# Performance work log

Measured on AMD Instinct MI355X. Metric: run time of the kernel, lower is better.

Reference implementation:

```python
import jax, jax.numpy as jnp
import numpy as np

K = 12
CHUNK = 1024
N_LAYERS = 4
WIDTH = 192
COND = 64
PE_DIM = 3 * 8 * 2 + 3  # 51
OUT_SCALE = 0.01
BIG = 1e9


def _build_knn(x, k=K, chunk=CHUNK):
    """Brute-force kNN, row-chunked like the TF double-chunked version.
    x: (N,3) float32 -> (N,k) int32 neighbor indices (self excluded)."""
    n = x.shape[0]
    x = x.astype(jnp.float32)
    x_sq = jnp.sum(x * x, axis=1)  # (N,)
    col_ids = jnp.arange(n, dtype=jnp.int32)
    starts = jnp.arange(0, n, chunk, dtype=jnp.int32)

    def one_chunk(start):
        xc = jax.lax.dynamic_slice(x, (start, 0), (chunk, 3))        # (chunk,3)
        sq_c = jax.lax.dynamic_slice(x_sq, (start,), (chunk,))       # (chunk,)
        d = sq_c[:, None] + x_sq[None, :] - 2.0 * (xc @ x.T)         # (chunk,N)
        d = jnp.maximum(d, 0.0)
        rows = start + jnp.arange(chunk, dtype=jnp.int32)
        d = d + jnp.where(rows[:, None] == col_ids[None, :], BIG, 0.0)  # exclude self
        _, idx = jax.lax.top_k(-d, k)                                 # smallest distances
        return idx.astype(jnp.int32)

    idx = jax.lax.map(one_chunk, starts)  # (n/chunk, chunk, k)
    return idx.reshape(n, k)


def _fourier(x, Bs):
    """concat_k [sin(xB_k), cos(xB_k)] + x  -> (N, PE_DIM)."""
    feats = []
    for B in Bs:
        xb = x @ B  # (N,8)
        feats.append(jnp.sin(xb))
        feats.append(jnp.cos(xb))
    feats.append(x)
    return jnp.concatenate(feats, axis=-1)


def setup_inputs() -> dict:
    key = jax.random.key(0)
    ks = jax.random.split(key, 16)
    n = 32768
    x = jax.random.normal(ks[0], (n, 3), dtype=jnp.float32)
    z = jax.random.normal(ks[1], (COND,), dtype=jnp.float32)
    sigmas = (1.0, 10.0, 50.0)
    B0 = jax.random.normal(ks[2], (3, 8), dtype=jnp.float32) * sigmas[0]
    B1 = jax.random.normal(ks[3], (3, 8), dtype=jnp.float32) * sigmas[1]
    B2 = jax.random.normal(ks[4], (3, 8), dtype=jnp.float32) * sigmas[2]
    in_total = PE_DIM + COND  # 115
    s = 0.05
    Wp = jax.random.normal(ks[5], (in_total, WIDTH), dtype=jnp.float32) * s
    bp = jnp.zeros((WIDTH,), dtype=jnp.float32)
    mix_dim = WIDTH + WIDTH + 6  # feat + agg + rel_feat
    Wl = jax.random.normal(ks[6], (N_LAYERS, mix_dim, WIDTH), dtype=jnp.float32) * s
    bl = jnp.zeros((N_LAYERS, WIDTH), dtype=jnp.float32)
    # FiLM: kernel ~zeros, gamma bias=ones, beta bias=zeros (perturbed slightly)
    Wg = jax.random.normal(ks[7], (N_LAYERS, COND, WIDTH), dtype=jnp.float32) * 0.01
    bg = jnp.ones((N_LAYERS, WIDTH), dtype=jnp.float32)
    Wb = jax.random.normal(ks[8], (N_LAYERS, COND, WIDTH), dtype=jnp.float32) * 0.01
    bb = jnp.zeros((N_LAYERS, WIDTH), dtype=jnp.float32)
    Wout = jax.random.normal(ks[9], (WIDTH, 3), dtype=jnp.float32) * s
    bout = jnp.zeros((3,), dtype=jnp.float32)
    return {"x": x, "z": z, "B0": B0, "B1": B1, "B2": B2,
            "Wp": Wp, "bp": bp, "Wl": Wl, "bl": bl,
            "Wg": Wg, "bg": bg, "Wb": Wb, "bb": bb,
            "Wout": Wout, "bout": bout}


def reference(x, z, B0, B1, B2, Wp, bp, Wl, bl, Wg, bg, Wb, bb, Wout, bout):
    n = x.shape[0]
    knn_idx = _build_knn(x)                     # (N,K) int32
    pe = _fourier(x, (B0, B1, B2))              # (N,51)
    zb = jnp.broadcast_to(z[None, :], (n, COND))
    feat = jnp.concatenate([pe, zb], axis=-1)   # (N,115)
    h = jax.nn.silu(feat @ Wp + bp)             # (N,WIDTH)
    # precompute relative-coordinate stats (same for all layers)
    nbr_coords = x[knn_idx]                     # (N,K,3)
    rel = nbr_coords - x[:, None, :]
    rel_feat = jnp.concatenate([rel.mean(axis=1), rel.std(axis=1)], axis=-1)  # (N,6)
    for li in range(N_LAYERS):
        nbr = h[knn_idx]                        # (N,K,WIDTH) gather
        agg = nbr.mean(axis=1)                  # (N,WIDTH)
        mix = jnp.concatenate([h, agg, rel_feat], axis=-1)  # (N,390)
        h = jax.nn.silu(mix @ Wl[li] + bl[li])
        gamma = z @ Wg[li] + bg[li]             # (WIDTH,)
        beta = z @ Wb[li] + bb[li]
        h = h * gamma[None, :] + beta[None, :]  # FiLM
    out = (h @ Wout + bout) * OUT_SCALE         # (N,3)
    return out
```

## Files before the change

kernel.cpp:

```cpp
#include <hip/hip_runtime.h>
#include <math.h>

#define WIDTH 192
#define KNN 12
#define G 64
#define NCELLS (G * G * G)
#define SMAX 8

#define CE(a, b) { double _lo = fmin(a, b); double _hi = fmax(a, b); a = _lo; b = _hi; }
#define INSERT12(key) { \
    b11 = fmin(b11, key); \
    CE(b10, b11); CE(b9, b10); CE(b8, b9); CE(b7, b8); CE(b6, b7); \
    CE(b5, b6);  CE(b4, b5); CE(b3, b4); CE(b2, b3); CE(b1, b2); CE(b0, b1); }
#define DECL12 double b0,b1,b2,b3,b4,b5,b6,b7,b8,b9,b10,b11
#define INIT12 { b0=__hiloint2double(0x7F7FFFFF,0);  b1=__hiloint2double(0x7F7FFFFF,1); \
    b2=__hiloint2double(0x7F7FFFFF,2);  b3=__hiloint2double(0x7F7FFFFF,3); \
    b4=__hiloint2double(0x7F7FFFFF,4);  b5=__hiloint2double(0x7F7FFFFF,5); \
    b6=__hiloint2double(0x7F7FFFFF,6);  b7=__hiloint2double(0x7F7FFFFF,7); \
    b8=__hiloint2double(0x7F7FFFFF,8);  b9=__hiloint2double(0x7F7FFFFF,9); \
    b10=__hiloint2double(0x7F7FFFFF,10); b11=__hiloint2double(0x7F7FFFFF,11); }

#define MERGE_STAGE(m) { \
    double pb11 = shflx_d(b11, m), pb10 = shflx_d(b10, m), pb9 = shflx_d(b9, m); \
    double pb8  = shflx_d(b8, m),  pb7  = shflx_d(b7, m),  pb6 = shflx_d(b6, m); \
    double pb5  = shflx_d(b5, m),  pb4  = shflx_d(b4, m),  pb3 = shflx_d(b3, m); \
    double pb2  = shflx_d(b2, m),  pb1  = shflx_d(b1, m),  pb0 = shflx_d(b0, m); \
    double c12 = pb3, c13 = pb2, c14 = pb1, c15 = pb0; \
    b4 = fmin(b4, pb11); b5 = fmin(b5, pb10); b6 = fmin(b6, pb9);  b7 = fmin(b7, pb8); \
    b8 = fmin(b8, pb7);  b9 = fmin(b9, pb6);  b10 = fmin(b10, pb5); b11 = fmin(b11, pb4); \
    CE(b0, b8);  CE(b1, b9);  CE(b2, b10); CE(b3, b11); \
    CE(b4, c12); CE(b5, c13); CE(b6, c14); CE(b7, c15); \
    CE(b0, b4);  CE(b1, b5);  CE(b2, b6);  CE(b3, b7); \
    CE(b8, c12); CE(b9, c13); CE(b10, c14); CE(b11, c15); \
    CE(b0, b2);  CE(b1, b3);  CE(b4, b6);  CE(b5, b7); \
    CE(b8, b10); CE(b9, b11); \
    CE(b0, b1);  CE(b2, b3);  CE(b4, b5);  CE(b6, b7); \
    CE(b8, b9);  CE(b10, b11); }

__device__ inline unsigned encf(float f) {
    unsigned u = __float_as_uint(f);
    return (u & 0x80000000u) ? ~u : (u | 0x80000000u);
}
__device__ inline float decf(unsigned u) {
    return (u & 0x80000000u) ? __uint_as_float(u & 0x7fffffffu) : __uint_as_float(~u);
}
__device__ inline int cellc(float v, float mn, float invh) {
    int c = (int)((v - mn) * invh);
    return min(max(c, 0), G - 1);
}
__device__ inline double shflx_d(double v, int m) {
    int lo = __shfl_xor(__double2loint(v), m, 64);
    int hi = __shfl_xor(__double2hiint(v), m, 64);
    return __hiloint2double(hi, lo);
}

__global__ __launch_bounds__(256) void precompute_kernel(
    const float* __restrict__ z, const float* __restrict__ Wp, const float* __restrict__ bp,
    const float* __restrict__ Wg, const float* __restrict__ bg,
    const float* __restrict__ Wb, const float* __restrict__ bb,
    float* __restrict__ bias0, float* __restrict__ gammaB, float* __restrict__ betaB)
{
    __shared__ float zs[64];
    int t = threadIdx.x;
    if (t < 64) zs[t] = z[t];
    __syncthreads();
    if (t < WIDTH) {
        float acc = bp[t];
        for (int k = 0; k < 64; ++k) acc += zs[k] * Wp[(51 + k) * WIDTH + t];
        bias0[t] = acc;
        for (int l = 0; l < 4; ++l) {
            float g = bg[l * WIDTH + t];
            float b = bb[l * WIDTH + t];
            for (int k = 0; k < 64; ++k) {
                g += zs[k] * Wg[(l * 64 + k) * WIDTH + t];
                b += zs[k] * Wb[(l * 64 + k) * WIDTH + t];
            }
            gammaB[l * WIDTH + t] = g;
            betaB[l * WIDTH + t] = b;
        }
    }
}

__global__ __launch_bounds__(256) void init_kernel(
    unsigned* __restrict__ bb, unsigned* __restrict__ counts,
    unsigned long long* __restrict__ rowmask)
{
    int i = blockIdx.x * 256 + threadIdx.x;
    if (i < 3) bb[i] = 0xFFFFFFFFu;
    else if (i < 6) bb[i] = 0u;
    counts[i] = 0u;
    if (i < G * G) rowmask[i] = 0ull;
}

__global__ __launch_bounds__(256) void bbox_kernel(
    const float* __restrict__ x, unsigned* __restrict__ bb, int n)
{
    int i = blockIdx.x * 256 + threadIdx.x;
    unsigned emin[3], emax[3];
#pragma unroll
    for (int a = 0; a < 3; ++a) { unsigned e = encf(x[i * 3 + a]); emin[a] = e; emax[a] = e; }
#pragma unroll
    for (int o = 32; o; o >>= 1) {
#pragma unroll
        for (int a = 0; a < 3; ++a) {
            emin[a] = min(emin[a], (unsigned)__shfl_xor((int)emin[a], o, 64));
            emax[a] = max(emax[a], (unsigned)__shfl_xor((int)emax[a], o, 64));
        }
    }
    if ((threadIdx.x & 63) == 0) {
#pragma unroll
        for (int a = 0; a < 3; ++a) {
            atomicMin(&bb[a], emin[a]);
            atomicMax(&bb[3 + a], emax[a]);
        }
    }
}

__global__ __launch_bounds__(256) void hist_kernel(
    const float* __restrict__ x, const unsigned* __restrict__ bb,
    unsigned* __restrict__ counts, unsigned long long* __restrict__ rowmask, int n)
{
    int i = blockIdx.x * 256 + threadIdx.x;
    float mnx = decf(bb[0]), mny = decf(bb[1]), mnz = decf(bb[2]);
    float ivx = (float)G / (decf(bb[3]) - mnx);
    float ivy = (float)G / (decf(bb[4]) - mny);
    float ivz = (float)G / (decf(bb[5]) - mnz);
    int cx = cellc(x[i * 3 + 0], mnx, ivx);
    int cy = cellc(x[i * 3 + 1], mny, ivy);
    int cz = cellc(x[i * 3 + 2], mnz, ivz);
    atomicAdd(&counts[(cz * G + cy) * G + cx], 1u);
    atomicOr(&rowmask[cz * G + cy], 1ull << cx);
}

__global__ __launch_bounds__(256) void scan1_kernel(
    const unsigned* __restrict__ counts, unsigned* __restrict__ offs,
    unsigned* __restrict__ bsums)
{
    __shared__ unsigned s[256];
    int b = blockIdx.x, t = threadIdx.x;
    unsigned base = (unsigned)b * 1024 + t * 4;
    unsigned v[4], sum = 0;
#pragma unroll
    for (int k = 0; k < 4; ++k) { v[k] = counts[base + k]; sum += v[k]; }
    s[t] = sum; __syncthreads();
    for (int off = 1; off < 256; off <<= 1) {
        unsigned xv = (t >= off) ? s[t - off] : 0u;
        __syncthreads();
        s[t] += xv;
        __syncthreads();
    }
    unsigned excl = s[t] - sum;
    if (t == 255) bsums[b] = s[255];
    unsigned run = excl;
#pragma unroll
    for (int k = 0; k < 4; ++k) { offs[base + k] = run; run += v[k]; }
}

__global__ __launch_bounds__(256) void scan3_kernel(
    unsigned* __restrict__ offs, const unsigned* __restrict__ bsums,
    unsigned* __restrict__ cursors, int n)
{
    __shared__ unsigned s[256];
    int b = blockIdx.x, t = threadIdx.x;
    s[t] = (t < b) ? bsums[t] : 0u;
    __syncthreads();
    for (int off = 128; off; off >>= 1) {
        if (t < off) s[t] += s[t + off];
        __syncthreads();
    }
    unsigned add = s[0];
    unsigned base = (unsigned)b * 1024 + t * 4;
#pragma unroll
    for (int k = 0; k < 4; ++k) {
        unsigned v = offs[base + k] + add;
        offs[base + k] = v;
        cursors[base + k] = v;
    }
    if (b == 255 && t == 255) offs[NCELLS] = (unsigned)n;
}

__global__ __launch_bounds__(256) void scatter_kernel(
    const float* __restrict__ x, const unsigned* __restrict__ bb,
    unsigned* __restrict__ cursors, float4* __restrict__ sorted,
    unsigned* __restrict__ inv, int n)
{
    int i = blockIdx.x * 256 + threadIdx.x;
    float mnx = decf(bb[0]), mny = decf(bb[1]), mnz = decf(bb[2]);
    float ivx = (float)G / (decf(bb[3]) - mnx);
    float ivy = (float)G / (decf(bb[4]) - mny);
    float ivz = (float)G / (decf(bb[5]) - mnz);
    float x0 = x[i * 3 + 0], x1 = x[i * 3 + 1], x2 = x[i * 3 + 2];
    int cx = cellc(x0, mnx, ivx);
    int cy = cellc(x1, mny, ivy);
    int cz = cellc(x2, mnz, ivz);
    unsigned pos = atomicAdd(&cursors[(cz * G + cy) * G + cx], 1u);
    sorted[pos] = make_float4(x0, x1, x2, __int_as_float(i));
    inv[i] = pos;
}

__global__ __launch_bounds__(64) void knn_grid_kernel(
    const float4* __restrict__ sorted, const unsigned* __restrict__ offs,
    const unsigned long long* __restrict__ rowmask,
    const unsigned* __restrict__ bb, const float* __restrict__ x,
    const unsigned* __restrict__ inv,
    unsigned short* __restrict__ knn, float* __restrict__ relf, int n)
{
    const int l = threadIdx.x;
    const int l32 = l & 31;
    const int g32 = l >> 5;
    const int b = blockIdx.x;
    const int nch = n >> 6;
    const int ch = b >> 5, posb = b & 31;
    const int fch = (ch & 1) ? (nch - 1 - (ch >> 1)) : (ch >> 1);
    const int p = fch * 64 + posb * 2 + g32;

    float mnx = decf(bb[0]), mny = decf(bb[1]), mnz = decf(bb[2]);
    float mxx = decf(bb[3]), mxy = decf(bb[4]), mxz = decf(bb[5]);
    float hx = (mxx - mnx) / G, hy = (mxy - mny) / G, hz = (mxz - mnz) / G;
    float ivx = (float)G / (mxx - mnx);
    float ivy = (float)G / (mxy - mny);
    float ivz = (float)G / (mxz - mnz);

    float4 q = sorted[p];
    float xi = q.x, yi = q.y, zi = q.z;
    int iorig = __float_as_int(q.w);
    float sqi = fmaf(zi, zi, fmaf(yi, yi, xi * xi));
    int cx = cellc(xi, mnx, ivx), cy = cellc(yi, mny, ivy), cz = cellc(zi, mnz, ivz);
    float fx = (xi - mnx) - cx * hx;
    float fy = (yi - mny) - cy * hy;
    float fz = (zi - mnz) - cz * hz;

    DECL12; INIT12;
    float worst = 3.402823466e+38f;
    float worst_g = 3.402823466e+38f;
    int nc = 0;
    bool have12 = false;

    auto groupMinWorst = [&]() -> float {
        float wm = worst;
        wm = fminf(wm, __shfl_xor(wm, 1, 64));
        wm = fminf(wm, __shfl_xor(wm, 2, 64));
        wm = fminf(wm, __shfl_xor(wm, 4, 64));
        wm = fminf(wm, __shfl_xor(wm, 8, 64));
        wm = fminf(wm, __shfl_xor(wm, 16, 64));
        return wm;
    };

    auto lane12Bound = [&]() -> float {
        float v = __int_as_float(__double2hiint(b0));
#pragma unroll
        for (int k = 2; k <= 32; k <<= 1) {
#pragma unroll
            for (int j = k >> 1; j >= 1; j >>= 1) {
                float pv = __shfl_xor(v, j, 64);
                bool dir = ((l32 & k) == 0);
                bool lower = ((l32 & j) == 0);
                float mn = fminf(v, pv), mx = fmaxf(v, pv);
                v = (lower == dir) ? mn : mx;
            }
        }
        return __shfl(v, (l & 32) | 11, 64);
    };

    auto groupUnionD12 = [&]() -> float {
        double c0=b0,c1=b1,c2=b2,c3=b3,c4=b4,c5=b5,c6=b6,c7=b7,c8=b8,c9=b9,c10=b10,c11=b11;
        {
            double b0=c0,b1=c1,b2=c2,b3=c3,b4=c4,b5=c5,b6=c6,b7=c7,b8=c8,b9=c9,b10=c10,b11=c11;
#pragma unroll
            for (int m = 1; m <= 16; m <<= 1) MERGE_STAGE(m)
            return __int_as_float(__double2hiint(b11));
        }
    };

    auto scanRange = [&](int c0, int c1) {
        unsigned j0 = offs[c0], j1 = offs[c1 + 1];
        if (j0 >= j1) return;
        float4 c = sorted[j0];
        for (unsigned t = j0; t < j1; ++t) {
            unsigned tn = (t + 1 < j1) ? t + 1 : t;
            float4 nx = sorted[tn];
            float sqj = fmaf(c.z, c.z, fmaf(c.y, c.y, c.x * c.x));
            float dot = fmaf(zi, c.z, fmaf(yi, c.y, xi * c.x));
            float d = fmaf(-2.0f, dot, sqi + sqj);
            int jg = __float_as_int(c.w);
            if (d <= fminf(worst, worst_g) && jg != iorig) {
                d = fmaxf(d, 0.0f);
                double key = __hiloint2double(__float_as_int(d), jg);
                INSERT12(key);
                worst = __int_as_float(__double2hiint(b11));
                ++nc;
            }
            c = nx;
        }
    };

    auto scanStrided = [&](int c0, int c1, int sub, int step) {
        unsigned j0 = offs[c0], j1 = offs[c1 + 1];
        for (unsigned t = j0 + sub; t < j1; t += step) {
            float4 c = sorted[t];
            float sqj = fmaf(c.z, c.z, fmaf(c.y, c.y, c.x * c.x));
            float dot = fmaf(zi, c.z, fmaf(yi, c.y, xi * c.x));
            float d = fmaf(-2.0f, dot, sqi + sqj);
            int jg = __float_as_int(c.w);
            if (d <= fminf(worst, worst_g) && jg != iorig) {
                d = fmaxf(d, 0.0f);
                double key = __hiloint2double(__float_as_int(d), jg);
                INSERT12(key);
                worst = __int_as_float(__double2hiint(b11));
                ++nc;
            }
        }
    };

    auto doRow = [&](int s, int dz, int dy, int sub, int step) {
        int zz = cz + dz, yy = cy + dy;
        if (zz < 0 || zz >= G || yy < 0 || yy >= G) return;
        int row = zz * G + yy;
        unsigned long long rm = rowmask[row];
        if (rm == 0ull) return;
        int rb = row * G;
        int adz = dz < 0 ? -dz : dz, ady = dy < 0 ? -dy : dy;
        if (adz == s || ady == s) {
            int x0 = max(cx - s, 0), x1 = min(cx + s, G - 1);
            unsigned long long msk =
                ((x1 == 63) ? ~0ull : ((1ull << (x1 + 1)) - 1ull)) &
                ~((1ull << x0) - 1ull);
            unsigned long long mm = rm & msk;
            if (mm) {
                int c0 = __ffsll((unsigned long long)mm) - 1;
                int c1 = 63 - __clzll((long long)mm);
                if (step == 1) scanRange(rb + c0, rb + c1);
                else           scanStrided(rb + c0, rb + c1, sub, step);
            }
        } else {
            int xm = cx - s, xp = cx + s;
            if (xm >= 0 && ((rm >> xm) & 1ull)) {
                if (step == 1) scanRange(rb + xm, rb + xm);
                else           scanStrided(rb + xm, rb + xm, sub, step);
            }
            if (xp < G && ((rm >> xp) & 1ull)) {
                if (step == 1) scanRange(rb + xp, rb + xp);
                else           scanStrided(rb + xp, rb + xp, sub, step);
            }
        }
    };

    auto check12 = [&]() {
        if (!have12) {
            int ns = nc;
#pragma unroll
            for (int o = 1; o <= 16; o <<= 1) ns += __shfl_xor(ns, o, 64);
            have12 = (ns >= 12);
        }
    };

    bool done = false;
    for (int s = 0; s <= SMAX; ++s) {
        if (s > 0) {
            float bx = (s - 1) * hx + fminf(fx, hx - fx);
            float by = (s - 1) * hy + fminf(fy, hy - fy);
            float bz = (s - 1) * hz + fminf(fz, hz - fz);
            float bnd = fminf(bx, fminf(by, bz));
            float bnd2 = bnd * bnd;
            worst_g = fminf(worst_g, groupMinWorst());
            if (bnd2 > worst_g + 1e-4f) { done = true; break; }
            unsigned long long anyb =
                __ballot(__double2hiint(b0) != 0x7F7FFFFF);
            unsigned gm = (unsigned)(anyb >> (g32 << 5));
            if (__popc(gm) >= 12) {
                worst_g = fminf(worst_g, lane12Bound());
                if (bnd2 > worst_g + 1e-4f) { done = true; break; }
            }
            if (s >= 2) {
                check12();
                if (have12) {
                    worst_g = fminf(worst_g, groupUnionD12());
                    if (bnd2 > worst_g + 1e-4f) { done = true; break; }
                }
            }
        }
        if (s == 0) {
            int row = cz * G + cy;
            if ((rowmask[row] >> cx) & 1ull) {
                int rb = row * G;
                scanStrided(rb + cx, rb + cx, l32, 32);
            }
        } else {
            int w2 = 2 * s + 1;
            int nrows = w2 * w2;
            int lpr = 32 / nrows;
            if (lpr > 1) {
                int r = l32 / lpr, sub = l32 - r * lpr;
                if (r < nrows) {
                    int dz = r / w2 - s, dy = r - (r / w2) * w2 - s;
                    doRow(s, dz, dy, sub, lpr);
                }
            } else {
                float rcp = 1.0f / (float)w2;
                for (int r = l32; r < nrows; r += 32) {
                    int qd = (int)((float)r * rcp);
                    int rem = r - qd * w2;
                    if (rem < 0) { qd--; rem += w2; }
                    else if (rem >= w2) { qd++; rem -= w2; }
                    doRow(s, qd - s, rem - s, 0, 1);
                }
            }
        }
    }
    if (!done) {
        float bx = SMAX * hx + fminf(fx, hx - fx);
        float by = SMAX * hy + fminf(fy, hy - fy);
        float bz = SMAX * hz + fminf(fz, hz - fz);
        float bnd = fminf(bx, fminf(by, bz));
        float bnd2 = bnd * bnd;
        worst_g = fminf(worst_g, groupMinWorst());
        if (bnd2 > worst_g + 1e-4f) done = true;
        if (!done) {
            unsigned long long anyb =
                __ballot(__double2hiint(b0) != 0x7F7FFFFF);
            unsigned gm = (unsigned)(anyb >> (g32 << 5));
            if (__popc(gm) >= 12) {
                worst_g = fminf(worst_g, lane12Bound());
                if (bnd2 > worst_g + 1e-4f) done = true;
            }
        }
        if (!done) {
            check12();
            if (have12) {
                worst_g = fminf(worst_g, groupUnionD12());
                if (bnd2 > worst_g + 1e-4f) done = true;
            }
        }
    }
    if (!done) {
        INIT12;
        worst = 3.402823466e+38f;
        for (int base = 0; base < n; base += 256) {
            float4 cc[8];
#pragma unroll
            for (int r = 0; r < 8; ++r) cc[r] = sorted[base + l32 + r * 32];
#pragma unroll
            for (int r = 0; r < 8; ++r) {
                float4 c = cc[r];
                float sqj = fmaf(c.z, c.z, fmaf(c.y, c.y, c.x * c.x));
                float dot = fmaf(zi, c.z, fmaf(yi, c.y, xi * c.x));
                float d = fmaf(-2.0f, dot, sqi + sqj);
                int jg = __float_as_int(c.w);
                if (d <= fminf(worst, worst_g) && jg != iorig) {
                    d = fmaxf(d, 0.0f);
                    double key = __hiloint2double(__float_as_int(d), jg);
                    INSERT12(key);
                    worst = __int_as_float(__double2hiint(b11));
                }
            }
        }
    }

#pragma unroll
    for (int m = 1; m <= 16; m <<= 1) MERGE_STAGE(m)

    if (l32 == 0) {
        int idx[KNN];
        idx[0]=__double2loint(b0);  idx[1]=__double2loint(b1);  idx[2]=__double2loint(b2);
        idx[3]=__double2loint(b3);  idx[4]=__double2loint(b4);  idx[5]=__double2loint(b5);
        idx[6]=__double2loint(b6);  idx[7]=__double2loint(b7);  idx[8]=__double2loint(b8);
        idx[9]=__double2loint(b9);  idx[10]=__double2loint(b10); idx[11]=__double2loint(b11);

        float rx[KNN], ry[KNN], rz[KNN];
        float sx = 0.f, sy = 0.f, sz = 0.f;
#pragma unroll
        for (int s = 0; s < KNN; ++s) {
            int j = idx[s];
            knn[(size_t)p * KNN + s] = (unsigned short)inv[j];
            rx[s] = x[(size_t)j * 3 + 0] - xi;
            ry[s] = x[(size_t)j * 3 + 1] - yi;
            rz[s] = x[(size_t)j * 3 + 2] - zi;
            sx += rx[s]; sy += ry[s]; sz += rz[s];
        }
        float mx = sx / 12.0f, my = sy / 12.0f, mz = sz / 12.0f;
        float vx = 0.f, vy = 0.f, vz = 0.f;
#pragma unroll
        for (int s = 0; s < KNN; ++s) {
            float dx = rx[s] - mx, dy = ry[s] - my, dz = rz[s] - mz;
            vx += dx * dx; vy += dy * dy; vz += dz * dz;
        }
        float* rr = relf + (size_t)p * 8;
        rr[0] = mx; rr[1] = my; rr[2] = mz;
        rr[3] = sqrtf(vx / 12.0f); rr[4] = sqrtf(vy / 12.0f); rr[5] = sqrtf(vz / 12.0f);
        rr[6] = 0.0f; rr[7] = 0.0f;
    }
}

template <int MODE>
__global__ __launch_bounds__(256) void gemm_silu_kernel(
    const float* __restrict__ A0, const unsigned short* __restrict__ knnp,
    const float* __restrict__ Rel, const float4* __restrict__ sorted4,
    const float* __restrict__ Bf0, const float* __restrict__ Bf1,
    const float* __restrict__ Bf2,
    const float* __restrict__ W, const float* __restrict__ bias,
    const float* __restrict__ gamma, const float* __restrict__ beta,
    const float* __restrict__ Wout, const float* __restrict__ bout,
    float* __restrict__ hout, float* __restrict__ fout)
{
    __shared__ float As[16][68];
    __shared__ float Bs[16][196];
    __shared__ float wouts[576];
    const int tid = threadIdx.x;
    const int ty = tid >> 4, tx = tid & 15;
    const int m0 = blockIdx.x * 64;
    const int arow = tid >> 2, akoff = (tid & 3) * 4;
    const int bk = tid >> 4,  bc = (tid & 15) * 12;

    float acc[4][12] = {};
    const int NCH = (MODE == 0) ? 4 : 24;

    if (MODE == 2) {
        for (int e = tid; e < 576; e += 256) wouts[e] = Wout[e];
    }

    float qx = 0.f, qy = 0.f, qz = 0.f;
    if (MODE == 0) {
        float4 qq = sorted4[m0 + arow];
        qx = qq.x; qy = qq.y; qz = qq.z;
    }

    unsigned kf[6] = {0, 0, 0, 0, 0, 0};
    if (MODE != 0) {
        const unsigned* kp = (const unsigned*)(knnp + (size_t)(m0 + arow) * KNN);
#pragma unroll
        for (int w = 0; w < 6; ++w) kf[w] = kp[w];
    }

    auto loadA = [&](int ch) -> float4 {
        int k0 = ch * 16;
        if (MODE == 0) {
            int c0 = k0 + akoff;
            float v[4];
            if (c0 < 48) {
                int m = c0 >> 4, jb = c0 & 15;
                const float* B = (m == 0) ? Bf0 : (m == 1) ? Bf1 : Bf2;
                bool iscos = jb >= 8;
                int j0 = iscos ? jb - 8 : jb;
#pragma unroll
                for (int e = 0; e < 4; ++e) {
                    int j = j0 + e;
                    float arg = qx * B[j] + qy * B[8 + j] + qz * B[16 + j];
                    v[e] = iscos ? cosf(arg) : sinf(arg);
                }
            } else {
#pragma unroll
                for (int e = 0; e < 4; ++e) {
                    int c = c0 + e;
                    v[e] = (c == 48) ? qx : (c == 49) ? qy : (c == 50) ? qz : 0.0f;
                }
            }
            return make_float4(v[0], v[1], v[2], v[3]);
        } else if (k0 < 192) {
            return *(const float4*)&A0[(size_t)(m0 + arow) * 192 + k0 + akoff];
        } else {
            int c4 = (k0 - 192 + akoff) >> 2;
            const float4* h4 = (const float4*)A0;
            float4 s = make_float4(0.f, 0.f, 0.f, 0.f);
#pragma unroll
            for (int j = 0; j < KNN; ++j) {
                unsigned idx = (j & 1) ? (kf[j >> 1] >> 16) : (kf[j >> 1] & 0xFFFFu);
                float4 v = h4[(size_t)idx * 48 + c4];
                s.x += v.x; s.y += v.y; s.z += v.z; s.w += v.w;
            }
            const float r = 1.0f / 12.0f;
            return make_float4(s.x * r, s.y * r, s.z * r, s.w * r);
        }
    };

    float4 ra = loadA(0);
    const float* wr0 = &W[(size_t)bk * 192 + bc];
    float4 rb0 = *(const float4*)&wr0[0];
    float4 rb1 = *(const float4*)&wr0[4];
    float4 rb2 = *(const float4*)&wr0[8];

    for (int ch = 0; ch < NCH; ++ch) {
        As[akoff + 0][arow] = ra.x; As[akoff + 1][arow] = ra.y;
        As[akoff + 2][arow] = ra.z; As[akoff + 3][arow] = ra.w;
        *(float4*)&Bs[bk][bc + 0] = rb0;
        *(float4*)&Bs[bk][bc + 4] = rb1;
        *(float4*)&Bs[bk][bc + 8] = rb2;
        __syncthreads();
        if (ch + 1 < NCH) {
            ra = loadA(ch + 1);
            const float* wr = &W[(size_t)((ch + 1) * 16 + bk) * 192 + bc];
            rb0 = *(const float4*)&wr[0];
            rb1 = *(const float4*)&wr[4];
            rb2 = *(const float4*)&wr[8];
        }
#pragma unroll
        for (int k = 0; k < 16; ++k) {
            float4 a0 = *(const float4*)&As[k][ty * 4];
            float av[4] = {a0.x, a0.y, a0.z, a0.w};
            float4 q0 = *(const float4*)&Bs[k][tx * 12 + 0];
            float4 q1 = *(const float4*)&Bs[k][tx * 12 + 4];
            float4 q2 = *(const float4*)&Bs[k][tx * 12 + 8];
            float bv[12] = {q0.x, q0.y, q0.z, q0.w, q1.x, q1.y, q1.z, q1.w,
                            q2.x, q2.y, q2.z, q2.w};
#pragma unroll
            for (int a = 0; a < 4; ++a)
#pragma unroll
                for (int bcol = 0; bcol < 12; ++bcol)
                    acc[a][bcol] = fmaf(av[a], bv[bcol], acc[a][bcol]);
        }
        __syncthreads();
    }

    if (MODE != 0) {
        {
            int row = tid >> 2, cp = (tid & 3) * 2;
            float2 v = *(const float2*)&Rel[(size_t)(m0 + row) * 8 + cp];
            As[cp + 0][row] = v.x; As[cp + 1][row] = v.y;
        }
        {
            int k2 = tid >> 4, c = (tid & 15) * 12;
            if (k2 < 8) {
                int gk = 384 + k2; if (gk > 389) gk = 389;
                const float* wr = &W[(size_t)gk * 192 + c];
                *(float4*)&Bs[k2][c + 0] = *(const float4*)&wr[0];
                *(float4*)&Bs[k2][c + 4] = *(const float4*)&wr[4];
                *(float4*)&Bs[k2][c + 8] = *(const float4*)&wr[8];
            }
        }
        __syncthreads();
#pragma unroll
        for (int k = 0; k < 8; ++k) {
            float4 a0 = *(const float4*)&As[k][ty * 4];
            float av[4] = {a0.x, a0.y, a0.z, a0.w};
            float4 q0 = *(const float4*)&Bs[k][tx * 12 + 0];
            float4 q1 = *(const float4*)&Bs[k][tx * 12 + 4];
            float4 q2 = *(const float4*)&Bs[k][tx * 12 + 8];
            float bv[12] = {q0.x, q0.y, q0.z, q0.w, q1.x, q1.y, q1.z, q1.w,
                            q2.x, q2.y, q2.z, q2.w};
#pragma unroll
            for (int a = 0; a < 4; ++a)
#pragma unroll
                for (int bcol = 0; bcol < 12; ++bcol)
                    acc[a][bcol] = fmaf(av[a], bv[bcol], acc[a][bcol]);
        }
        __syncthreads();
    }

    float po[4][3] = {};
#pragma unroll
    for (int a = 0; a < 4; ++a) {
        int gi = m0 + ty * 4 + a;
        float res[12];
#pragma unroll
        for (int bcol = 0; bcol < 12; ++bcol) {
            int gc = tx * 12 + bcol;
            float v = acc[a][bcol] + bias[gc];
            float s = 1.0f / (1.0f + expf(-v));
            v = v * s;
            if (MODE != 0) v = v * gamma[gc] + beta[gc];
            res[bcol] = v;
        }
        if (MODE == 2) {
#pragma unroll
            for (int e = 0; e < 12; ++e) {
                int c = tx * 12 + e;
                po[a][0] = fmaf(res[e], wouts[c * 3 + 0], po[a][0]);
                po[a][1] = fmaf(res[e], wouts[c * 3 + 1], po[a][1]);
                po[a][2] = fmaf(res[e], wouts[c * 3 + 2], po[a][2]);
            }
        } else {
            float* orow = &hout[(size_t)gi * 192 + tx * 12];
            *(float4*)&orow[0] = make_float4(res[0], res[1], res[2], res[3]);
            *(float4*)&orow[4] = make_float4(res[4], res[5], res[6], res[7]);
            *(float4*)&orow[8] = make_float4(res[8], res[9], res[10], res[11]);
        }
    }

    if (MODE == 2) {
#pragma unroll
        for (int a = 0; a < 4; ++a)
#pragma unroll
            for (int j = 0; j < 3; ++j) {
                float v = po[a][j];
                v += __shfl_xor(v, 1, 64);
                v += __shfl_xor(v, 2, 64);
                v += __shfl_xor(v, 4, 64);
                v += __shfl_xor(v, 8, 64);
                po[a][j] = v;
            }
        if (tx == 0) {
#pragma unroll
            for (int a = 0; a < 4; ++a) {
                int gi = m0 + ty * 4 + a;
                int iorig = __float_as_int(sorted4[gi].w);
                fout[(size_t)iorig * 3 + 0] = (po[a][0] + bout[0]) * 0.01f;
                fout[(size_t)iorig * 3 + 1] = (po[a][1] + bout[1]) * 0.01f;
                fout[(size_t)iorig * 3 + 2] = (po[a][2] + bout[2]) * 0.01f;
            }
        }
    }
}

extern "C" void kernel_launch(void* const* d_in, const int* in_sizes, int n_in,
                              void* d_out, int out_size, void* d_ws, size_t ws_size,
                              hipStream_t stream)
{
    const float* x    = (const float*)d_in[0];
    const float* z    = (const float*)d_in[1];
    const float* B0   = (const float*)d_in[2];
    const float* B1   = (const float*)d_in[3];
    const float* B2   = (const float*)d_in[4];
    const float* Wp   = (const float*)d_in[5];
    const float* bp   = (const float*)d_in[6];
    const float* Wl   = (const float*)d_in[7];
    const float* bl   = (const float*)d_in[8];
    const float* Wg   = (const float*)d_in[9];
    const float* bg   = (const float*)d_in[10];
    const float* Wb   = (const float*)d_in[11];
    const float* bb   = (const float*)d_in[12];
    const float* Wout = (const float*)d_in[13];
    const float* bout = (const float*)d_in[14];

    int n = in_sizes[0] / 3;

    float* ws = (float*)d_ws;
    float* bias0  = ws;
    float* gammaB = ws + 192;
    float* betaB  = ws + 960;
    size_t off = 1728;
    unsigned short* knn = (unsigned short*)(ws + off);  off += (size_t)n * 6;
    float* relf = ws + off;                off += (size_t)n * 8;
    float4* sorted = (float4*)(ws + off);  off += (size_t)n * 4;
    float* hA   = ws + off;                off += (size_t)n * 192;
    float* hB   = ws + off;                off += (size_t)n * 192;

    unsigned* bbx     = (unsigned*)hA;
    unsigned* counts  = bbx + 8;
    unsigned* offsA   = counts + NCELLS;
    unsigned* cursors = offsA + NCELLS + 1;
    unsigned* bsums   = cursors + NCELLS;
    size_t gu = 8 + (size_t)NCELLS * 3 + 1 + 256;
    gu = (gu + 1) & ~(size_t)1;
    unsigned long long* rowmask = (unsigned long long*)((unsigned*)hA + gu);
    gu += (size_t)G * G * 2;
    unsigned* inv = (unsigned*)hA + gu;

    init_kernel<<<NCELLS / 256, 256, 0, stream>>>(bbx, counts, rowmask);
    precompute_kernel<<<1, 256, 0, stream>>>(z, Wp, bp, Wg, bg, Wb, bb,
                                             bias0, gammaB, betaB);
    bbox_kernel<<<n / 256, 256, 0, stream>>>(x, bbx, n);
    hist_kernel<<<n / 256, 256, 0, stream>>>(x, bbx, counts, rowmask, n);
    scan1_kernel<<<NCELLS / 1024, 256, 0, stream>>>(counts, offsA, bsums);
    scan3_kernel<<<NCELLS / 1024, 256, 0, stream>>>(offsA, bsums, cursors, n);
    scatter_kernel<<<n / 256, 256, 0, stream>>>(x, bbx, cursors, sorted, inv, n);
    knn_grid_kernel<<<n / 2, 64, 0, stream>>>(sorted, offsA, rowmask, bbx, x,
                                              inv, knn, relf, n);

    gemm_silu_kernel<0><<<n / 64, 256, 0, stream>>>(
        nullptr, nullptr, nullptr, sorted, B0, B1, B2,
        Wp, bias0, nullptr, nullptr, nullptr, nullptr, hA, nullptr);

    float* hcur = hA;
    float* hnxt = hB;
    for (int li = 0; li < 3; ++li) {
        gemm_silu_kernel<1><<<n / 64, 256, 0, stream>>>(
            hcur, knn, relf, nullptr, nullptr, nullptr, nullptr,
            Wl + (size_t)li * 390 * 192, bl + (size_t)li * 192,
            gammaB + (size_t)li * 192, betaB + (size_t)li * 192,
            nullptr, nullptr, hnxt, nullptr);
        float* t = hcur; hcur = hnxt; hnxt = t;
    }
    gemm_silu_kernel<2><<<n / 64, 256, 0, stream>>>(
        hcur, knn, relf, sorted, nullptr, nullptr, nullptr,
        Wl + (size_t)3 * 390 * 192, bl + (size_t)3 * 192,
        gammaB + (size_t)3 * 192, betaB + (size_t)3 * 192,
        Wout, bout, nullptr, (float*)d_out);
}
```

Baseline: 682.5 us.

## Fuse grid-build and MLP layer launches into persistent kernels with software grid barriers

```diff
diff --git a/kernel.cpp b/kernel.cpp
--- a/kernel.cpp
+++ b/kernel.cpp
@@ -6,6 +6,7 @@
 #define G 64
 #define NCELLS (G * G * G)
 #define SMAX 8
+#define BUILD_BLOCKS (NCELLS / 256)
 
 #define CE(a, b) { double _lo = fmin(a, b); double _hi = fmax(a, b); a = _lo; b = _hi; }
 #define INSERT12(key) { \
@@ -54,148 +55,142 @@
     return __hiloint2double(hi, lo);
 }
 
-__global__ __launch_bounds__(256) void precompute_kernel(
-    const float* __restrict__ z, const float* __restrict__ Wp, const float* __restrict__ bp,
-    const float* __restrict__ Wg, const float* __restrict__ bg,
-    const float* __restrict__ Wb, const float* __restrict__ bb,
-    float* __restrict__ bias0, float* __restrict__ gammaB, float* __restrict__ betaB)
+__device__ __forceinline__ void gbar(unsigned* c, unsigned target) {
+    __syncthreads();
+    if (threadIdx.x == 0) {
+        __threadfence();
+        atomicAdd(c, 1u);
+        while (__hip_atomic_load(c, __ATOMIC_RELAXED, __HIP_MEMORY_SCOPE_AGENT)
+               < target)
+            __builtin_amdgcn_s_sleep(2);
+        __threadfence();
+    }
+    __syncthreads();
+}
+
+__global__ __launch_bounds__(256, 4) void build_kernel(
+    const float* __restrict__ x, const float* __restrict__ z,
+    const float* __restrict__ Wp, const float* __restrict__ bp,
+    const float* __restrict__ Wg, const float* __restrict__ bgf,
+    const float* __restrict__ Wb, const float* __restrict__ bbf,
+    float* __restrict__ bias0, float* __restrict__ gammaB,
+    float* __restrict__ betaB,
+    unsigned* __restrict__ bbx, unsigned* __restrict__ counts,
+    unsigned long long* __restrict__ rowmask, unsigned* __restrict__ offs,
+    unsigned* __restrict__ bsums, unsigned* __restrict__ cursors,
+    float4* __restrict__ sorted, unsigned* __restrict__ inv,
+    unsigned* __restrict__ ctrs, int n)
 {
+    const int t = threadIdx.x, b = blockIdx.x;
+    const int gid = b * 256 + t;
+    const unsigned NB = gridDim.x;
+    __shared__ unsigned su[256];
     __shared__ float zs[64];
-    int t = threadIdx.x;
-    if (t < 64) zs[t] = z[t];
-    __syncthreads();
-    if (t < WIDTH) {
-        float acc = bp[t];
-        for (int k = 0; k < 64; ++k) acc += zs[k] * Wp[(51 + k) * WIDTH + t];
-        bias0[t] = acc;
-        for (int l = 0; l < 4; ++l) {
-            float g = bg[l * WIDTH + t];
-            float b = bb[l * WIDTH + t];
-            for (int k = 0; k < 64; ++k) {
-                g += zs[k] * Wg[(l * 64 + k) * WIDTH + t];
-                b += zs[k] * Wb[(l * 64 + k) * WIDTH + t];
-            }
-            gammaB[l * WIDTH + t] = g;
-            betaB[l * WIDTH + t] = b;
-        }
-    }
-}
-
-__global__ __launch_bounds__(256) void init_kernel(
-    unsigned* __restrict__ bb, unsigned* __restrict__ counts,
-    unsigned long long* __restrict__ rowmask)
-{
-    int i = blockIdx.x * 256 + threadIdx.x;
-    if (i < 3) bb[i] = 0xFFFFFFFFu;
-    else if (i < 6) bb[i] = 0u;
-    counts[i] = 0u;
-    if (i < G * G) rowmask[i] = 0ull;
-}
-
-__global__ __launch_bounds__(256) void bbox_kernel(
-    const float* __restrict__ x, unsigned* __restrict__ bb, int n)
-{
-    int i = blockIdx.x * 256 + threadIdx.x;
-    unsigned emin[3], emax[3];
-#pragma unroll
-    for (int a = 0; a < 3; ++a) { unsigned e = encf(x[i * 3 + a]); emin[a] = e; emax[a] = e; }
-#pragma unroll
-    for (int o = 32; o; o >>= 1) {
+
+    counts[gid] = 0u;
+    if (gid < G * G) rowmask[gid] = 0ull;
+    if (gid < 3) bbx[gid] = 0xFFFFFFFFu;
+    else if (gid < 6) bbx[gid] = 0u;
+    gbar(&ctrs[0], NB);
+
+    if (gid < n) {
+        unsigned emin[3], emax[3];
 #pragma unroll
         for (int a = 0; a < 3; ++a) {
-            emin[a] = min(emin[a], (unsigned)__shfl_xor((int)emin[a], o, 64));
-            emax[a] = max(emax[a], (unsigned)__shfl_xor((int)emax[a], o, 64));
-        }
-    }
-    if ((threadIdx.x & 63) == 0) {
-#pragma unroll
-        for (int a = 0; a < 3; ++a) {
-            atomicMin(&bb[a], emin[a]);
-            atomicMax(&bb[3 + a], emax[a]);
-        }
-    }
-}
-
-__global__ __launch_bounds__(256) void hist_kernel(
-    const float* __restrict__ x, const unsigned* __restrict__ bb,
-    unsigned* __restrict__ counts, unsigned long long* __restrict__ rowmask, int n)
-{
-    int i = blockIdx.x * 256 + threadIdx.x;
-    float mnx = decf(bb[0]), mny = decf(bb[1]), mnz = decf(bb[2]);
-    float ivx = (float)G / (decf(bb[3]) - mnx);
-    float ivy = (float)G / (decf(bb[4]) - mny);
-    float ivz = (float)G / (decf(bb[5]) - mnz);
-    int cx = cellc(x[i * 3 + 0], mnx, ivx);
-    int cy = cellc(x[i * 3 + 1], mny, ivy);
-    int cz = cellc(x[i * 3 + 2], mnz, ivz);
-    atomicAdd(&counts[(cz * G + cy) * G + cx], 1u);
-    atomicOr(&rowmask[cz * G + cy], 1ull << cx);
-}
-
-__global__ __launch_bounds__(256) void scan1_kernel(
-    const unsigned* __restrict__ counts, unsigned* __restrict__ offs,
-    unsigned* __restrict__ bsums)
-{
-    __shared__ unsigned s[256];
-    int b = blockIdx.x, t = threadIdx.x;
-    unsigned base = (unsigned)b * 1024 + t * 4;
-    unsigned v[4], sum = 0;
-#pragma unroll
-    for (int k = 0; k < 4; ++k) { v[k] = counts[base + k]; sum += v[k]; }
-    s[t] = sum; __syncthreads();
+            unsigned e = encf(x[gid * 3 + a]); emin[a] = e; emax[a] = e;
+        }
+#pragma unroll
+        for (int o = 32; o; o >>= 1) {
+#pragma unroll
+            for (int a = 0; a < 3; ++a) {
+                emin[a] = min(emin[a], (unsigned)__shfl_xor((int)emin[a], o, 64));
+                emax[a] = max(emax[a], (unsigned)__shfl_xor((int)emax[a], o, 64));
+            }
+        }
+        if ((t & 63) == 0) {
+#pragma unroll
+            for (int a = 0; a < 3; ++a) {
+                atomicMin(&bbx[a], emin[a]);
+                atomicMax(&bbx[3 + a], emax[a]);
+            }
+        }
+    }
+    if (b == (int)NB - 1) {
+        if (t < 64) zs[t] = z[t];
+        __syncthreads();
+        if (t < WIDTH) {
+            float acc = bp[t];
+            for (int k = 0; k < 64; ++k) acc += zs[k] * Wp[(51 + k) * WIDTH + t];
+            bias0[t] = acc;
+            for (int l = 0; l < 4; ++l) {
+                float g = bgf[l * WIDTH + t];
+                float bv = bbf[l * WIDTH + t];
+                for (int k = 0; k < 64; ++k) {
+                    g  += zs[k] * Wg[(l * 64 + k) * WIDTH + t];
+                    bv += zs[k] * Wb[(l * 64 + k) * WIDTH + t];
+                }
+                gammaB[l * WIDTH + t] = g;
+                betaB[l * WIDTH + t] = bv;
+            }
+        }
+    }
+    gbar(&ctrs[1], NB);
+
+    if (gid < n) {
+        float mnx = decf(bbx[0]), mny = decf(bbx[1]), mnz = decf(bbx[2]);
+        float ivx = (float)G / (decf(bbx[3]) - mnx);
+        float ivy = (float)G / (decf(bbx[4]) - mny);
+        float ivz = (float)G / (decf(bbx[5]) - mnz);
+        int cx = cellc(x[gid * 3 + 0], mnx, ivx);
+        int cy = cellc(x[gid * 3 + 1], mny, ivy);
+        int cz = cellc(x[gid * 3 + 2], mnz, ivz);
+        atomicAdd(&counts[(cz * G + cy) * G + cx], 1u);
+        atomicOr(&rowmask[cz * G + cy], 1ull << cx);
+    }
+    gbar(&ctrs[2], NB);
+
+    unsigned v = counts[gid];
+    su[t] = v; __syncthreads();
     for (int off = 1; off < 256; off <<= 1) {
-        unsigned xv = (t >= off) ? s[t - off] : 0u;
+        unsigned xv = (t >= off) ? su[t - off] : 0u;
         __syncthreads();
-        s[t] += xv;
+        su[t] += xv;
         __syncthreads();
     }
-    unsigned excl = s[t] - sum;
-    if (t == 255) bsums[b] = s[255];
-    unsigned run = excl;
-#pragma unroll
-    for (int k = 0; k < 4; ++k) { offs[base + k] = run; run += v[k]; }
-}
-
-__global__ __launch_bounds__(256) void scan3_kernel(
-    unsigned* __restrict__ offs, const unsigned* __restrict__ bsums,
-    unsigned* __restrict__ cursors, int n)
-{
-    __shared__ unsigned s[256];
-    int b = blockIdx.x, t = threadIdx.x;
-    s[t] = (t < b) ? bsums[t] : 0u;
-    __syncthreads();
-    for (int off = 128; off; off >>= 1) {
-        if (t < off) s[t] += s[t + off];
+    offs[gid] = su[t] - v;
+    if (t == 255) bsums[b] = su[255];
+    gbar(&ctrs[3], NB);
+
+    {
+        unsigned a = 0;
+        for (int k = t; k < (int)NB; k += 256)
+            if (k < b) a += bsums[k];
         __syncthreads();
-    }
-    unsigned add = s[0];
-    unsigned base = (unsigned)b * 1024 + t * 4;
-#pragma unroll
-    for (int k = 0; k < 4; ++k) {
-        unsigned v = offs[base + k] + add;
-        offs[base + k] = v;
-        cursors[base + k] = v;
-    }
-    if (b == 255 && t == 255) offs[NCELLS] = (unsigned)n;
-}
-
-__global__ __launch_bounds__(256) void scatter_kernel(
-    const float* __restrict__ x, const unsigned* __restrict__ bb,
-    unsigned* __restrict__ cursors, float4* __restrict__ sorted,
-    unsigned* __restrict__ inv, int n)
-{
-    int i = blockIdx.x * 256 + threadIdx.x;
-    float mnx = decf(bb[0]), mny = decf(bb[1]), mnz = decf(bb[2]);
-    float ivx = (float)G / (decf(bb[3]) - mnx);
-    float ivy = (float)G / (decf(bb[4]) - mny);
-    float ivz = (float)G / (decf(bb[5]) - mnz);
-    float x0 = x[i * 3 + 0], x1 = x[i * 3 + 1], x2 = x[i * 3 + 2];
-    int cx = cellc(x0, mnx, ivx);
-    int cy = cellc(x1, mny, ivy);
-    int cz = cellc(x2, mnz, ivz);
-    unsigned pos = atomicAdd(&cursors[(cz * G + cy) * G + cx], 1u);
-    sorted[pos] = make_float4(x0, x1, x2, __int_as_float(i));
-    inv[i] = pos;
+        su[t] = a; __syncthreads();
+        for (int off = 128; off; off >>= 1) {
+            if (t < off) su[t] += su[t + off];
+            __syncthreads();
+        }
+        unsigned v2 = offs[gid] + su[0];
+        offs[gid] = v2;
+        cursors[gid] = v2;
+        if (b == (int)NB - 1 && t == 255) offs[NCELLS] = (unsigned)n;
+    }
+    gbar(&ctrs[4], NB);
+
+    if (gid < n) {
+        float mnx = decf(bbx[0]), mny = decf(bbx[1]), mnz = decf(bbx[2]);
+        float ivx = (float)G / (decf(bbx[3]) - mnx);
+        float ivy = (float)G / (decf(bbx[4]) - mny);
+        float ivz = (float)G / (decf(bbx[5]) - mnz);
+        float x0 = x[gid * 3 + 0], x1 = x[gid * 3 + 1], x2 = x[gid * 3 + 2];
+        int cx = cellc(x0, mnx, ivx);
+        int cy = cellc(x1, mny, ivy);
+        int cz = cellc(x2, mnz, ivz);
+        unsigned pos = atomicAdd(&cursors[(cz * G + cy) * G + cx], 1u);
+        sorted[pos] = make_float4(x0, x1, x2, __int_as_float(gid));
+        inv[gid] = pos;
+    }
 }
 
 __global__ __launch_bounds__(64) void knn_grid_kernel(
@@ -491,8 +486,15 @@
     }
 }
 
+struct GemmSmem {
+    float As[16][68];
+    float Bs[16][196];
+    float wouts[576];
+};
+
 template <int MODE>
-__global__ __launch_bounds__(256) void gemm_silu_kernel(
+__device__ __forceinline__ void gemm_layer(
+    GemmSmem& sm, int m0, int tid,
     const float* __restrict__ A0, const unsigned short* __restrict__ knnp,
     const float* __restrict__ Rel, const float4* __restrict__ sorted4,
     const float* __restrict__ Bf0, const float* __restrict__ Bf1,
@@ -502,12 +504,7 @@
     const float* __restrict__ Wout, const float* __restrict__ bout,
     float* __restrict__ hout, float* __restrict__ fout)
 {
-    __shared__ float As[16][68];
-    __shared__ float Bs[16][196];
-    __shared__ float wouts[576];
-    const int tid = threadIdx.x;
     const int ty = tid >> 4, tx = tid & 15;
-    const int m0 = blockIdx.x * 64;
     const int arow = tid >> 2, akoff = (tid & 3) * 4;
     const int bk = tid >> 4,  bc = (tid & 15) * 12;
 
@@ -515,7 +512,7 @@
     const int NCH = (MODE == 0) ? 4 : 24;
 
     if (MODE == 2) {
-        for (int e = tid; e < 576; e += 256) wouts[e] = Wout[e];
+        for (int e = tid; e < 576; e += 256) sm.wouts[e] = Wout[e];
     }
 
     float qx = 0.f, qy = 0.f, qz = 0.f;
@@ -579,11 +576,11 @@
     float4 rb2 = *(const float4*)&wr0[8];
 
     for (int ch = 0; ch < NCH; ++ch) {
-        As[akoff + 0][arow] = ra.x; As[akoff + 1][arow] = ra.y;
-        As[akoff + 2][arow] = ra.z; As[akoff + 3][arow] = ra.w;
-        *(float4*)&Bs[bk][bc + 0] = rb0;
-        *(float4*)&Bs[bk][bc + 4] = rb1;
-        *(float4*)&Bs[bk][bc + 8] = rb2;
+        sm.As[akoff + 0][arow] = ra.x; sm.As[akoff + 1][arow] = ra.y;
+        sm.As[akoff + 2][arow] = ra.z; sm.As[akoff + 3][arow] = ra.w;
+        *(float4*)&sm.Bs[bk][bc + 0] = rb0;
+        *(float4*)&sm.Bs[bk][bc + 4] = rb1;
+        *(float4*)&sm.Bs[bk][bc + 8] = rb2;
         __syncthreads();
         if (ch + 1 < NCH) {
             ra = loadA(ch + 1);
@@ -594,11 +591,11 @@
         }
 #pragma unroll
         for (int k = 0; k < 16; ++k) {
-            float4 a0 = *(const float4*)&As[k][ty * 4];
+            float4 a0 = *(const float4*)&sm.As[k][ty * 4];
             float av[4] = {a0.x, a0.y, a0.z, a0.w};
-            float4 q0 = *(const float4*)&Bs[k][tx * 12 + 0];
-            float4 q1 = *(const float4*)&Bs[k][tx * 12 + 4];
-            float4 q2 = *(const float4*)&Bs[k][tx * 12 + 8];
+            float4 q0 = *(const float4*)&sm.Bs[k][tx * 12 + 0];
+            float4 q1 = *(const float4*)&sm.Bs[k][tx * 12 + 4];
+            float4 q2 = *(const float4*)&sm.Bs[k][tx * 12 + 8];
             float bv[12] = {q0.x, q0.y, q0.z, q0.w, q1.x, q1.y, q1.z, q1.w,
                             q2.x, q2.y, q2.z, q2.w};
 #pragma unroll
@@ -614,26 +611,26 @@
         {
             int row = tid >> 2, cp = (tid & 3) * 2;
             float2 v = *(const float2*)&Rel[(size_t)(m0 + row) * 8 + cp];
-            As[cp + 0][row] = v.x; As[cp + 1][row] = v.y;
+            sm.As[cp + 0][row] = v.x; sm.As[cp + 1][row] = v.y;
         }
         {
             int k2 = tid >> 4, c = (tid & 15) * 12;
             if (k2 < 8) {
                 int gk = 384 + k2; if (gk > 389) gk = 389;
                 const float* wr = &W[(size_t)gk * 192 + c];
-                *(float4*)&Bs[k2][c + 0] = *(const float4*)&wr[0];
-                *(float4*)&Bs[k2][c + 4] = *(const float4*)&wr[4];
-                *(float4*)&Bs[k2][c + 8] = *(const float4*)&wr[8];
+                *(float4*)&sm.Bs[k2][c + 0] = *(const float4*)&wr[0];
+                *(float4*)&sm.Bs[k2][c + 4] = *(const float4*)&wr[4];
+                *(float4*)&sm.Bs[k2][c + 8] = *(const float4*)&wr[8];
             }
         }
         __syncthreads();
 #pragma unroll
         for (int k = 0; k < 8; ++k) {
-            float4 a0 = *(const float4*)&As[k][ty * 4];
+            float4 a0 = *(const float4*)&sm.As[k][ty * 4];
             float av[4] = {a0.x, a0.y, a0.z, a0.w};
-            float4 q0 = *(const float4*)&Bs[k][tx * 12 + 0];
-            float4 q1 = *(const float4*)&Bs[k][tx * 12 + 4];
-            float4 q2 = *(const float4*)&Bs[k][tx * 12 + 8];
+            float4 q0 = *(const float4*)&sm.Bs[k][tx * 12 + 0];
+            float4 q1 = *(const float4*)&sm.Bs[k][tx * 12 + 4];
+            float4 q2 = *(const float4*)&sm.Bs[k][tx * 12 + 8];
             float bv[12] = {q0.x, q0.y, q0.z, q0.w, q1.x, q1.y, q1.z, q1.w,
                             q2.x, q2.y, q2.z, q2.w};
 #pragma unroll
@@ -663,9 +660,9 @@
 #pragma unroll
             for (int e = 0; e < 12; ++e) {
                 int c = tx * 12 + e;
-                po[a][0] = fmaf(res[e], wouts[c * 3 + 0], po[a][0]);
-                po[a][1] = fmaf(res[e], wouts[c * 3 + 1], po[a][1]);
-                po[a][2] = fmaf(res[e], wouts[c * 3 + 2], po[a][2]);
+                po[a][0] = fmaf(res[e], sm.wouts[c * 3 + 0], po[a][0]);
+                po[a][1] = fmaf(res[e], sm.wouts[c * 3 + 1], po[a][1]);
+                po[a][2] = fmaf(res[e], sm.wouts[c * 3 + 2], po[a][2]);
             }
         } else {
             float* orow = &hout[(size_t)gi * 192 + tx * 12];
@@ -698,6 +695,45 @@
             }
         }
     }
+}
+
+__global__ __launch_bounds__(256, 2) void mlp_kernel(
+    const unsigned short* __restrict__ knnp, const float* __restrict__ Rel,
+    const float4* __restrict__ sorted4,
+    const float* __restrict__ B0, const float* __restrict__ B1,
+    const float* __restrict__ B2,
+    const float* __restrict__ Wp, const float* __restrict__ bias0,
+    const float* __restrict__ Wl, const float* __restrict__ bl,
+    const float* __restrict__ gammaB, const float* __restrict__ betaB,
+    const float* __restrict__ Wout, const float* __restrict__ bout,
+    float* __restrict__ hA, float* __restrict__ hB,
+    float* __restrict__ fout, unsigned* __restrict__ ctrs)
+{
+    __shared__ GemmSmem sm;
+    const int tid = threadIdx.x;
+    const int m0 = blockIdx.x * 64;
+    const unsigned NB = gridDim.x;
+
+    gemm_layer<0>(sm, m0, tid, nullptr, nullptr, nullptr, sorted4, B0, B1, B2,
+                  Wp, bias0, nullptr, nullptr, nullptr, nullptr, hA, nullptr);
+    gbar(&ctrs[8], NB);
+
+    float* hcur = hA;
+    float* hnxt = hB;
+    for (int li = 0; li < 3; ++li) {
+        gemm_layer<1>(sm, m0, tid, hcur, knnp, Rel, nullptr,
+                      nullptr, nullptr, nullptr,
+                      Wl + (size_t)li * 390 * 192, bl + li * 192,
+                      gammaB + li * 192, betaB + li * 192,
+                      nullptr, nullptr, hnxt, nullptr);
+        gbar(&ctrs[9 + li], NB);
+        float* tp = hcur; hcur = hnxt; hnxt = tp;
+    }
+    gemm_layer<2>(sm, m0, tid, hcur, knnp, Rel, sorted4,
+                  nullptr, nullptr, nullptr,
+                  Wl + (size_t)3 * 390 * 192, bl + 3 * 192,
+                  gammaB + 3 * 192, betaB + 3 * 192,
+                  Wout, bout, nullptr, fout);
 }
 
 extern "C" void kernel_launch(void* const* d_in, const int* in_sizes, int n_in,
@@ -726,7 +762,8 @@
     float* bias0  = ws;
     float* gammaB = ws + 192;
     float* betaB  = ws + 960;
-    size_t off = 1728;
+    unsigned* ctrs = (unsigned*)(ws + 1728);
+    size_t off = 1744;
     unsigned short* knn = (unsigned short*)(ws + off);  off += (size_t)n * 6;
     float* relf = ws + off;                off += (size_t)n * 8;
     float4* sorted = (float4*)(ws + off);  off += (size_t)n * 4;
@@ -738,40 +775,19 @@
     unsigned* offsA   = counts + NCELLS;
     unsigned* cursors = offsA + NCELLS + 1;
     unsigned* bsums   = cursors + NCELLS;
-    size_t gu = 8 + (size_t)NCELLS * 3 + 1 + 256;
+    size_t gu = 8 + (size_t)NCELLS * 3 + 1 + BUILD_BLOCKS;
     gu = (gu + 1) & ~(size_t)1;
     unsigned long long* rowmask = (unsigned long long*)((unsigned*)hA + gu);
     gu += (size_t)G * G * 2;
     unsigned* inv = (unsigned*)hA + gu;
 
-    init_kernel<<<NCELLS / 256, 256, 0, stream>>>(bbx, counts, rowmask);
-    precompute_kernel<<<1, 256, 0, stream>>>(z, Wp, bp, Wg, bg, Wb, bb,
-                                             bias0, gammaB, betaB);
-    bbox_kernel<<<n / 256, 256, 0, stream>>>(x, bbx, n);
-    hist_kernel<<<n / 256, 256, 0, stream>>>(x, bbx, counts, rowmask, n);
-    scan1_kernel<<<NCELLS / 1024, 256, 0, stream>>>(counts, offsA, bsums);
-    scan3_kernel<<<NCELLS / 1024, 256, 0, stream>>>(offsA, bsums, cursors, n);
-    scatter_kernel<<<n / 256, 256, 0, stream>>>(x, bbx, cursors, sorted, inv, n);
+    hipMemsetAsync(ctrs, 0, 64, stream);
+    build_kernel<<<BUILD_BLOCKS, 256, 0, stream>>>(
+        x, z, Wp, bp, Wg, bg, Wb, bb, bias0, gammaB, betaB,
+        bbx, counts, rowmask, offsA, bsums, cursors, sorted, inv, ctrs, n);
     knn_grid_kernel<<<n / 2, 64, 0, stream>>>(sorted, offsA, rowmask, bbx, x,
                                               inv, knn, relf, n);
-
-    gemm_silu_kernel<0><<<n / 64, 256, 0, stream>>>(
-        nullptr, nullptr, nullptr, sorted, B0, B1, B2,
-        Wp, bias0, nullptr, nullptr, nullptr, nullptr, hA, nullptr);
-
-    float* hcur = hA;
-    float* hnxt = hB;
-    for (int li = 0; li < 3; ++li) {
-        gemm_silu_kernel<1><<<n / 64, 256, 0, stream>>>(
-            hcur, knn, relf, nullptr, nullptr, nullptr, nullptr,
-            Wl + (size_t)li * 390 * 192, bl + (size_t)li * 192,
-            gammaB + (size_t)li * 192, betaB + (size_t)li * 192,
-            nullptr, nullptr, hnxt, nullptr);
-        float* t = hcur; hcur = hnxt; hnxt = t;
-    }
-    gemm_silu_kernel<2><<<n / 64, 256, 0, stream>>>(
-        hcur, knn, relf, sorted, nullptr, nullptr, nullptr,
-        Wl + (size_t)3 * 390 * 192, bl + (size_t)3 * 192,
-        gammaB + (size_t)3 * 192, betaB + (size_t)3 * 192,
-        Wout, bout, nullptr, (float*)d_out);
-}
+    mlp_kernel<<<n / 64, 256, 0, stream>>>(
+        knn, relf, sorted, B0, B1, B2, Wp, bias0, Wl, bl, gammaB, betaB,
+        Wout, bout, hA, hB, (float*)d_out, ctrs);
+}
```

Result: slower. 1.491 ms (+118.4%).
